# Kernel optimization log

Measured on AMD Instinct MI355X. Metric: run time of the kernel, lower is better.

## Reference

```python
import jax, jax.numpy as jnp
import numpy as np

INF = 1e10  # stands in for +inf in fp32-safe squared-distance field


def _dt1d_sq(f):
    """Exact 1D squared Euclidean distance transform along the last axis.
    f: (..., N) squared-distance field (0 on seeds, INF elsewhere).
    D[..., i] = min_j (i-j)^2 + f[..., j]  (brute-force lower envelope, exact).
    Uses lax.map over output index i to avoid an (..., N, N) intermediate.
    """
    N = f.shape[-1]
    idx = jnp.arange(N)

    def body(i):
        return jnp.min(f + ((i - idx) ** 2).astype(f.dtype), axis=-1)

    out = jax.lax.map(body, idx)  # (N, ...)
    return jnp.moveaxis(out, 0, -1)


def _edt(mask):
    """scipy.ndimage.distance_transform_edt(1 - mask) per (b, c):
    Euclidean distance to nearest mask==1 pixel; all-zeros if channel empty.
    mask: (B, C, H, W) binary float.
    """
    f = jnp.where(mask > 0.5, 0.0, INF)
    d = _dt1d_sq(f)                              # sweep along W
    d = _dt1d_sq(jnp.swapaxes(d, -1, -2))        # sweep along H
    d = jnp.sqrt(jnp.swapaxes(d, -1, -2))
    empty = jnp.sum(mask, axis=(-1, -2), keepdims=True) == 0
    return jnp.where(empty, 0.0, d)


def _boundary(x):
    """|2D laplacian| per channel with zero padding=1. x: (B, C, H, W)."""
    xp = jnp.pad(x, ((0, 0), (0, 0), (1, 1), (1, 1)))
    lap = (xp[:, :, :-2, 1:-1] + xp[:, :, 2:, 1:-1]
           + xp[:, :, 1:-1, :-2] + xp[:, :, 1:-1, 2:] - 4.0 * x)
    return jnp.abs(lap)


def setup_inputs() -> dict:
    key = jax.random.key(0)
    k1, k2 = jax.random.split(key)
    B, C, H, W = 8, 4, 256, 256
    pred = jax.random.normal(k1, (B, C, H, W), dtype=jnp.float32)
    target = jax.random.randint(k2, (B, H, W), 0, C, dtype=jnp.int64)
    return {"pred": pred, "target": target}


def reference(pred, target):
    C = pred.shape[1]
    p = jax.nn.softmax(pred, axis=1)                       # (B,C,H,W)
    t1h = jax.nn.one_hot(target, C, axis=1, dtype=p.dtype) # (B,C,H,W)
    target_dist = _edt(t1h)
    pred_boundary = _boundary(p)
    loss = jnp.sum(pred_boundary * target_dist) / jnp.sum(pred_boundary)
    return loss
```

## Files before the change

kernel.cpp:

```cpp
#include <hip/hip_runtime.h>

#define NB 8
#define NC 4
#define NH 256
#define NW 256
#define HW (NH * NW)
#define CHW (NC * HW)
#define INFV 1e10f
#define TH 4
#define MAIN_BLOCKS (NB * (NH / TH))
#define WR (TH + 8)

__global__ __launch_bounds__(256) void k_edt_w(const int* __restrict__ tgt,
                                               unsigned short* __restrict__ D16) {
    int bh = blockIdx.x;
    int i  = threadIdx.x;
    int wv = i >> 6;
    int ln = i & 63;

    int tv = tgt[(size_t)bh * NW + i];

    __shared__ unsigned long long mk[NC][4];
    #pragma unroll
    for (int c = 0; c < NC; ++c) {
        unsigned long long m = __ballot(tv == c);
        if (ln == 0) mk[c][wv] = m;
    }
    __syncthreads();

    unsigned long long le = (ln == 63) ? ~0ull : ((1ull << (ln + 1)) - 1ull);
    unsigned long long ge = ~0ull << ln;

    unsigned short res[NC];
    #pragma unroll
    for (int c = 0; c < NC; ++c) {
        int jl = -1000;
        #pragma unroll
        for (int k = 0; k < 4; ++k) {
            unsigned long long x = mk[c][k];
            x = (k > wv) ? 0ull : ((k == wv) ? (x & le) : x);
            if (x) jl = k * 64 + 63 - __clzll((long long)x);
        }
        int jr = 1000;
        #pragma unroll
        for (int k = 3; k >= 0; --k) {
            unsigned long long x = mk[c][k];
            x = (k < wv) ? 0ull : ((k == wv) ? (x & ge) : x);
            if (x) jr = k * 64 + __ffsll((unsigned long long)x) - 1;
        }
        int dl = i - jl;
        int dr = jr - i;
        int dd = min(dl, dr);
        res[c] = (dd > 255) ? (unsigned short)65535
                            : (unsigned short)(dd * dd);
    }

    int b = bh >> 8;
    int h = bh & 255;
    size_t o = (size_t)b * CHW + (size_t)h * NW + i;
    D16[o]          = res[0];
    D16[o + HW]     = res[1];
    D16[o + 2 * HW] = res[2];
    D16[o + 3 * HW] = res[3];
}

__device__ __forceinline__ void softmax4(const float* __restrict__ pred_b,
                                         int hw, float o[NC]) {
    float x0 = pred_b[hw];
    float x1 = pred_b[hw + HW];
    float x2 = pred_b[hw + 2 * HW];
    float x3 = pred_b[hw + 3 * HW];
    float m  = fmaxf(fmaxf(x0, x1), fmaxf(x2, x3));
    float e0 = __expf(x0 - m);
    float e1 = __expf(x1 - m);
    float e2 = __expf(x2 - m);
    float e3 = __expf(x3 - m);
    float inv = 1.0f / (e0 + e1 + e2 + e3);
    o[0] = e0 * inv; o[1] = e1 * inv; o[2] = e2 * inv; o[3] = e3 * inv;
}

__global__ __launch_bounds__(256) void k_main(const float* __restrict__ pred,
                                              const unsigned short* __restrict__ D16,
                                              float2* __restrict__ partial) {
    int blk  = blockIdx.x;
    int b    = blk >> 6;
    int tile = blk & 63;
    int h0   = tile * TH;
    int w    = threadIdx.x;

    const unsigned short* Db = D16 + (size_t)b * CHW + w;

    float win[WR][NC];
    #pragma unroll
    for (int k = 0; k < WR; ++k) {
        int j = h0 - 4 + k;
        bool ok = (unsigned)j < (unsigned)NH;
        #pragma unroll
        for (int c = 0; c < NC; ++c) {
            unsigned short u = ok ? Db[(size_t)c * HW + (j << 8)]
                                  : (unsigned short)65535;
            win[k][c] = (u > 65025) ? INFV : (float)u;
        }
    }

    const float* pred_b = pred + (size_t)b * CHW;

    float num = 0.0f, den = 0.0f;
    #pragma unroll
    for (int r = 0; r < TH; ++r) {
        int h  = h0 + r;
        int hw = (h << 8) + w;

        float pc[NC], pu[NC] = {0,0,0,0}, pd[NC] = {0,0,0,0},
              pl[NC] = {0,0,0,0}, pr[NC] = {0,0,0,0};
        softmax4(pred_b, hw, pc);
        if (h > 0)   softmax4(pred_b, hw - NW, pu);
        if (h < 255) softmax4(pred_b, hw + NW, pd);
        if (w > 0)   softmax4(pred_b, hw - 1,  pl);
        if (w < 255) softmax4(pred_b, hw + 1,  pr);

        #pragma unroll
        for (int c = 0; c < NC; ++c) {
            float lap = fabsf(pu[c] + pd[c] + pl[c] + pr[c] - 4.0f * pc[c]);

            float best = win[r + 4][c];
            #pragma unroll
            for (int dr = 1; dr <= 4; ++dr) {
                float rr = (float)(dr * dr);
                best = fminf(best, rr + win[r + 4 - dr][c]);
                best = fminf(best, rr + win[r + 4 + dr][c]);
            }

            if (best > 25.0f) {
                const unsigned short* f = Db + (size_t)c * HW;
                for (int r2 = 5; r2 < NH; ++r2) {
                    float rr = (float)(r2 * r2);
                    if (rr >= best) break;
                    int hu = h - r2, hd = h + r2;
                    if (hu >= 0) {
                        unsigned short u = f[hu << 8];
                        if (u <= 65025) best = fminf(best, rr + (float)u);
                    }
                    if (hd < NH) {
                        unsigned short u = f[hd << 8];
                        if (u <= 65025) best = fminf(best, rr + (float)u);
                    }
                }
            }

            float dv = (best > 1e8f) ? 0.0f : sqrtf(best);
            num += lap * dv;
            den += lap;
        }
    }

    #pragma unroll
    for (int off = 32; off > 0; off >>= 1) {
        num += __shfl_down(num, off);
        den += __shfl_down(den, off);
    }
    __shared__ float sn[4], sd[4];
    int lane = threadIdx.x & 63;
    int wvi  = threadIdx.x >> 6;
    if (lane == 0) { sn[wvi] = num; sd[wvi] = den; }
    __syncthreads();
    if (threadIdx.x == 0) {
        partial[blockIdx.x] = make_float2(sn[0] + sn[1] + sn[2] + sn[3],
                                          sd[0] + sd[1] + sd[2] + sd[3]);
    }
}

__global__ __launch_bounds__(256) void k_final(const float2* __restrict__ partial,
                                               float* __restrict__ out) {
    double n = 0.0, d = 0.0;
    for (int i = threadIdx.x; i < MAIN_BLOCKS; i += 256) {
        float2 v = partial[i];
        n += (double)v.x;
        d += (double)v.y;
    }
    #pragma unroll
    for (int off = 32; off > 0; off >>= 1) {
        n += __shfl_down(n, off);
        d += __shfl_down(d, off);
    }
    __shared__ double snd[4], sdd[4];
    int lane = threadIdx.x & 63;
    int wv   = threadIdx.x >> 6;
    if (lane == 0) { snd[wv] = n; sdd[wv] = d; }
    __syncthreads();
    if (threadIdx.x == 0) {
        double nn = snd[0] + snd[1] + snd[2] + snd[3];
        double dd = sdd[0] + sdd[1] + sdd[2] + sdd[3];
        out[0] = (float)(nn / dd);
    }
}

extern "C" void kernel_launch(void* const* d_in, const int* in_sizes, int n_in,
                              void* d_out, int out_size, void* d_ws, size_t ws_size,
                              hipStream_t stream) {
    const float* pred = (const float*)d_in[0];
    const int*   tgt  = (const int*)d_in[1];
    float*       out  = (float*)d_out;

    unsigned short* D16     = (unsigned short*)d_ws;
    float2*         partial = (float2*)((char*)d_ws + (size_t)NB * CHW * 2);

    k_edt_w<<<NB * NH,     256, 0, stream>>>(tgt, D16);
    k_main <<<MAIN_BLOCKS, 256, 0, stream>>>(pred, D16, partial);
    k_final<<<1,           256, 0, stream>>>(partial, out);
}
```

Before: 26.10 us.

## Store W-pass distances column-major with halo padding and stage softmax in LDS

The first pass now handles 4 rows per block and writes the per-row distance field transposed: column-major per (b,c,w), with 4 padding entries holding the sentinel at each end. This lets the main kernel load its 12-row vertical window with three 8-byte vector loads per channel instead of strided 2-byte loads. The long vertical search becomes contiguous per thread. The main kernel also computes softmax once per pixel of a (TH+2)x(NW+2) halo tile in shared memory, replacing five recomputations per pixel. The trade-offs are writes with a stride of one column per thread in the first pass, a larger workspace, and added LDS use.

```diff
diff --git a/kernel.cpp b/kernel.cpp
--- a/kernel.cpp
+++ b/kernel.cpp
@@ -8,60 +8,76 @@
 #define CHW (NC * HW)
 #define INFV 1e10f
 #define TH 4
+#define HP 264
 #define MAIN_BLOCKS (NB * (NH / TH))
-#define WR (TH + 8)
 
 __global__ __launch_bounds__(256) void k_edt_w(const int* __restrict__ tgt,
-                                               unsigned short* __restrict__ D16) {
-    int bh = blockIdx.x;
-    int i  = threadIdx.x;
-    int wv = i >> 6;
-    int ln = i & 63;
-
-    int tv = tgt[(size_t)bh * NW + i];
-
-    __shared__ unsigned long long mk[NC][4];
-    #pragma unroll
-    for (int c = 0; c < NC; ++c) {
-        unsigned long long m = __ballot(tv == c);
-        if (ln == 0) mk[c][wv] = m;
+                                               unsigned short* __restrict__ Dt) {
+    int blk  = blockIdx.x;
+    int b    = blk >> 6;
+    int tile = blk & 63;
+    int h0   = tile * TH;
+    int t    = threadIdx.x;
+    int wv   = t >> 6;
+    int ln   = t & 63;
+
+    __shared__ unsigned long long mk[TH][NC][4];
+
+    int tv[TH];
+    #pragma unroll
+    for (int r = 0; r < TH; ++r)
+        tv[r] = tgt[((size_t)b * NH + h0 + r) * NW + t];
+
+    #pragma unroll
+    for (int r = 0; r < TH; ++r) {
+        #pragma unroll
+        for (int c = 0; c < NC; ++c) {
+            unsigned long long m = __ballot(tv[r] == c);
+            if (ln == 0) mk[r][c][wv] = m;
+        }
     }
     __syncthreads();
 
     unsigned long long le = (ln == 63) ? ~0ull : ((1ull << (ln + 1)) - 1ull);
     unsigned long long ge = ~0ull << ln;
 
-    unsigned short res[NC];
     #pragma unroll
     for (int c = 0; c < NC; ++c) {
-        int jl = -1000;
-        #pragma unroll
-        for (int k = 0; k < 4; ++k) {
-            unsigned long long x = mk[c][k];
-            x = (k > wv) ? 0ull : ((k == wv) ? (x & le) : x);
-            if (x) jl = k * 64 + 63 - __clzll((long long)x);
-        }
-        int jr = 1000;
-        #pragma unroll
-        for (int k = 3; k >= 0; --k) {
-            unsigned long long x = mk[c][k];
-            x = (k < wv) ? 0ull : ((k == wv) ? (x & ge) : x);
-            if (x) jr = k * 64 + __ffsll((unsigned long long)x) - 1;
-        }
-        int dl = i - jl;
-        int dr = jr - i;
-        int dd = min(dl, dr);
-        res[c] = (dd > 255) ? (unsigned short)65535
-                            : (unsigned short)(dd * dd);
-    }
-
-    int b = bh >> 8;
-    int h = bh & 255;
-    size_t o = (size_t)b * CHW + (size_t)h * NW + i;
-    D16[o]          = res[0];
-    D16[o + HW]     = res[1];
-    D16[o + 2 * HW] = res[2];
-    D16[o + 3 * HW] = res[3];
+        unsigned short q[TH];
+        #pragma unroll
+        for (int r = 0; r < TH; ++r) {
+            int jl = -1000;
+            #pragma unroll
+            for (int k = 0; k < 4; ++k) {
+                unsigned long long x = mk[r][c][k];
+                x = (k > wv) ? 0ull : ((k == wv) ? (x & le) : x);
+                if (x) jl = k * 64 + 63 - __clzll((long long)x);
+            }
+            int jr = 1000;
+            #pragma unroll
+            for (int k = 3; k >= 0; --k) {
+                unsigned long long x = mk[r][c][k];
+                x = (k < wv) ? 0ull : ((k == wv) ? (x & ge) : x);
+                if (x) jr = k * 64 + __ffsll((unsigned long long)x) - 1;
+            }
+            int dd = min(t - jl, jr - t);
+            q[r] = (dd > 255) ? (unsigned short)65535
+                              : (unsigned short)(dd * dd);
+        }
+        uint2 pk;
+        pk.x = (unsigned)q[0] | ((unsigned)q[1] << 16);
+        pk.y = (unsigned)q[2] | ((unsigned)q[3] << 16);
+        unsigned short* colp = Dt + ((size_t)(b * NC + c) * NW + t) * HP;
+        *(uint2*)(colp + 4 + h0) = pk;
+        if (tile == 0) {
+            uint2 s; s.x = 0xFFFFFFFFu; s.y = 0xFFFFFFFFu;
+            *(uint2*)(colp) = s;
+        }
+        if (tile == 63) {
+            uint2 s; s.x = 0xFFFFFFFFu; s.y = 0xFFFFFFFFu;
+            *(uint2*)(colp + 260) = s;
+        }
+    }
 }
 
 __device__ __forceinline__ void softmax4(const float* __restrict__ pred_b,
@@ -80,7 +96,7 @@
 }
 
 __global__ __launch_bounds__(256) void k_main(const float* __restrict__ pred,
-                                              const unsigned short* __restrict__ D16,
+                                              const unsigned short* __restrict__ Dt,
                                               float2* __restrict__ partial) {
     int blk  = blockIdx.x;
     int b    = blk >> 6;
@@ -88,40 +104,51 @@
     int h0   = tile * TH;
     int w    = threadIdx.x;
 
-    const unsigned short* Db = D16 + (size_t)b * CHW + w;
-
-    float win[WR][NC];
-    #pragma unroll
-    for (int k = 0; k < WR; ++k) {
-        int j = h0 - 4 + k;
-        bool ok = (unsigned)j < (unsigned)NH;
+    const float* pred_b = pred + (size_t)b * CHW;
+
+    float win[TH + 8][NC];
+    #pragma unroll
+    for (int c = 0; c < NC; ++c) {
+        const unsigned short* colp =
+            Dt + ((size_t)(b * NC + c) * NW + w) * HP + 4 + h0;
+        uint2 v0 = *(const uint2*)(colp - 4);
+        uint2 v1 = *(const uint2*)(colp);
+        uint2 v2 = *(const uint2*)(colp + 4);
+        unsigned v[6] = {v0.x, v0.y, v1.x, v1.y, v2.x, v2.y};
+        #pragma unroll
+        for (int k = 0; k < 6; ++k) {
+            unsigned a = v[k] & 0xFFFFu;
+            unsigned d = v[k] >> 16;
+            win[2 * k][c]     = (a > 65025u) ? INFV : (float)a;
+            win[2 * k + 1][c] = (d > 65025u) ? INFV : (float)d;
+        }
+    }
+
+    __shared__ float ps[NC][TH + 2][NW + 2];
+    for (int pos = threadIdx.x; pos < (TH + 2) * (NW + 2); pos += 256) {
+        int row = pos / (NW + 2);
+        int col = pos - row * (NW + 2);
+        int gy  = h0 - 1 + row;
+        int gx  = col - 1;
+        float o[NC] = {0.0f, 0.0f, 0.0f, 0.0f};
+        if ((unsigned)gy < (unsigned)NH && (unsigned)gx < (unsigned)NW)
+            softmax4(pred_b, (gy << 8) + gx, o);
+        ps[0][row][col] = o[0];
+        ps[1][row][col] = o[1];
+        ps[2][row][col] = o[2];
+        ps[3][row][col] = o[3];
+    }
+    __syncthreads();
+
+    float num = 0.0f, den = 0.0f;
+    #pragma unroll
+    for (int r = 0; r < TH; ++r) {
+        int h = h0 + r;
         #pragma unroll
         for (int c = 0; c < NC; ++c) {
-            unsigned short u = ok ? Db[(size_t)c * HW + (j << 8)]
-                                  : (unsigned short)65535;
-            win[k][c] = (u > 65025) ? INFV : (float)u;
-        }
-    }
-
-    const float* pred_b = pred + (size_t)b * CHW;
-
-    float num = 0.0f, den = 0.0f;
-    #pragma unroll
-    for (int r = 0; r < TH; ++r) {
-        int h  = h0 + r;
-        int hw = (h << 8) + w;
-
-        float pc[NC], pu[NC] = {0,0,0,0}, pd[NC] = {0,0,0,0},
-              pl[NC] = {0,0,0,0}, pr[NC] = {0,0,0,0};
-        softmax4(pred_b, hw, pc);
-        if (h > 0)   softmax4(pred_b, hw - NW, pu);
-        if (h < 255) softmax4(pred_b, hw + NW, pd);
-        if (w > 0)   softmax4(pred_b, hw - 1,  pl);
-        if (w < 255) softmax4(pred_b, hw + 1,  pr);
-
-        #pragma unroll
-        for (int c = 0; c < NC; ++c) {
-            float lap = fabsf(pu[c] + pd[c] + pl[c] + pr[c] - 4.0f * pc[c]);
+            float lap = fabsf(ps[c][r][w + 1] + ps[c][r + 2][w + 1]
+                            + ps[c][r + 1][w] + ps[c][r + 1][w + 2]
+                            - 4.0f * ps[c][r + 1][w + 1]);
 
             float best = win[r + 4][c];
             #pragma unroll
@@ -132,17 +159,18 @@
             }
 
             if (best > 25.0f) {
-                const unsigned short* f = Db + (size_t)c * HW;
+                const unsigned short* f =
+                    Dt + ((size_t)(b * NC + c) * NW + w) * HP + 4;
                 for (int r2 = 5; r2 < NH; ++r2) {
                     float rr = (float)(r2 * r2);
                     if (rr >= best) break;
                     int hu = h - r2, hd = h + r2;
                     if (hu >= 0) {
-                        unsigned short u = f[hu << 8];
+                        unsigned short u = f[hu];
                         if (u <= 65025) best = fminf(best, rr + (float)u);
                     }
                     if (hd < NH) {
-                        unsigned short u = f[hd << 8];
+                        unsigned short u = f[hd];
                         if (u <= 65025) best = fminf(best, rr + (float)u);
                     }
                 }
@@ -202,10 +230,11 @@
     const int*   tgt  = (const int*)d_in[1];
     float*       out  = (float*)d_out;
 
-    unsigned short* D16     = (unsigned short*)d_ws;
-    float2*         partial = (float2*)((char*)d_ws + (size_t)NB * CHW * 2);
-
-    k_edt_w<<<NB * NH,     256, 0, stream>>>(tgt, D16);
-    k_main <<<MAIN_BLOCKS, 256, 0, stream>>>(pred, D16, partial);
-    k_final<<<1,           256, 0, stream>>>(partial, out);
-}
+    unsigned short* Dt      = (unsigned short*)d_ws;
+    float2*         partial = (float2*)((char*)d_ws
+                              + (size_t)NB * NC * NW * HP * sizeof(unsigned short));
+
+    k_edt_w<<<NB * (NH / TH), 256, 0, stream>>>(tgt, Dt);
+    k_main <<<MAIN_BLOCKS,    256, 0, stream>>>(pred, Dt, partial);
+    k_final<<<1,              256, 0, stream>>>(partial, out);
+}
```

Result: slower. 31.84 us (+22.0%).
